# Kernel optimization log

Hardware: AMD Instinct MI355X
Metric: run time of the kernel (lower is better)

Reference implementation:

```python
import jax, jax.numpy as jnp
import numpy as np

EPS = 1e-6  # epsilon used to snap near-zero plane distances (Moller-style robustness)


def _interval(p, d):
    """Interval of the intersection line covered by a triangle.
    p: [..., 3] projections of the 3 vertices onto the intersection-line axis.
    d: [..., 3] signed distances of the 3 vertices to the other triangle's plane.
    Returns (tmin, tmax); invalid (non-straddling) -> (+inf, -inf).
    """
    nxt = jnp.array([1, 2, 0])
    di, dj = d, d[..., nxt]
    pi, pj = p, p[..., nxt]
    # edge crosses the plane iff endpoint distances have opposite signs
    # (or exactly one endpoint lies on the plane)
    valid = (di * dj <= 0) & ~((di == 0) & (dj == 0))
    denom = di - dj
    t = pi + (pj - pi) * di / jnp.where(denom == 0, 1.0, denom)
    tmin = jnp.min(jnp.where(valid, t, jnp.inf), axis=-1)
    tmax = jnp.max(jnp.where(valid, t, -jnp.inf), axis=-1)
    return tmin, tmax


def _pairwise_intersect(T):
    """Moller-style triangle-triangle intersection test for all N^2 pairs.
    T: [N, 3, 3] triangle soup. Returns bool [N, N].
    """
    N = T.shape[0]
    n = jnp.cross(T[:, 1] - T[:, 0], T[:, 2] - T[:, 0])   # [N,3] plane normals
    d = -jnp.sum(n * T[:, 0], axis=-1)                      # [N] plane offsets
    # signed distances: verts of triangle b to plane of triangle u (dv), and vice versa (du)
    dv = jnp.einsum('bvc,nc->bnv', T, n) + d[None, :, None]  # [N,N,3]
    du = jnp.einsum('nvc,bc->bnv', T, n) + d[:, None, None]  # [N,N,3]
    dv = jnp.where(jnp.abs(dv) < EPS, 0.0, dv)
    du = jnp.where(jnp.abs(du) < EPS, 0.0, du)
    # all vertices strictly on one side -> no intersection
    ssv = jnp.all(dv > 0, -1) | jnp.all(dv < 0, -1)
    ssu = jnp.all(du > 0, -1) | jnp.all(du < 0, -1)
    # direction of plane-plane intersection line; project onto its dominant axis
    D = jnp.cross(n[:, None, :], n[None, :, :])              # [N,N,3]
    ax = jnp.argmax(jnp.abs(D), axis=-1)                     # [N,N]
    idx = jnp.broadcast_to(ax[..., None, None], (N, N, 3, 1))
    pv = jnp.take_along_axis(jnp.broadcast_to(T[:, None], (N, N, 3, 3)), idx, -1)[..., 0]
    pu = jnp.take_along_axis(jnp.broadcast_to(T[None, :], (N, N, 3, 3)), idx, -1)[..., 0]
    t0v, t1v = _interval(pv, dv)
    t0u, t1u = _interval(pu, du)
    overlap = jnp.maximum(t0v, t0u) <= jnp.minimum(t1v, t1u)
    return ~ssv & ~ssu & overlap


def setup_inputs() -> dict:
    key = jax.random.key(0)
    triangles = jax.random.normal(key, (2048, 3, 3), dtype=jnp.float32)
    return {"triangles": triangles}


def reference(triangles):
    # CPU extension produces the strictly-upper-triangular pairwise matrix;
    # the torch wrapper symmetrizes it and adds the identity.
    N = triangles.shape[0]
    M = _pairwise_intersect(triangles).astype(jnp.float32)
    S = jnp.triu(M, 1)
    return S + S.T + jnp.eye(N, dtype=jnp.float32)
```

## Files before the change

kernel.cpp:

```cpp
#include <hip/hip_runtime.h>
#include <math.h>


static constexpr float EPS_SNAP = 1e-6f;

__device__ __forceinline__ float snapz(float x) {
    return (fabsf(x) < EPS_SNAP) ? 0.0f : x;
}

__device__ __forceinline__ void tri_interval(const float p[3], const float d[3],
                                             float& tmin, float& tmax) {
#pragma clang fp contract(off)
    tmin = INFINITY;
    tmax = -INFINITY;
#pragma unroll
    for (int e = 0; e < 3; ++e) {
        const int i0 = e;
        const int i1 = (e + 1) % 3;
        const float di = d[i0], dj = d[i1];
        const float pi = p[i0], pj = p[i1];
        const bool valid = (di * dj <= 0.0f) && !((di == 0.0f) && (dj == 0.0f));
        const float denom = di - dj;
        const float dsafe = (denom == 0.0f) ? 1.0f : denom;
        const float t = pi + ((pj - pi) * di) / dsafe;
        if (valid) {
            tmin = fminf(tmin, t);
            tmax = fmaxf(tmax, t);
        }
    }
}

__global__ __launch_bounds__(256) void tri_pairs_kernel(
    const float* __restrict__ tri, float* __restrict__ out, int n)
{
#pragma clang fp contract(off)
    const int j = blockIdx.x * 64 + threadIdx.x;
    const int i = blockIdx.y * 4 + threadIdx.y;
    if (i >= n || j >= n) return;

    const float* __restrict__ A = tri + (size_t)i * 9;
    const float* __restrict__ B = tri + (size_t)j * 9;

    float Av[9], Bv[9];
#pragma unroll
    for (int k = 0; k < 9; ++k) { Av[k] = A[k]; Bv[k] = B[k]; }

    const float ae1x = Av[3] - Av[0], ae1y = Av[4] - Av[1], ae1z = Av[5] - Av[2];
    const float ae2x = Av[6] - Av[0], ae2y = Av[7] - Av[1], ae2z = Av[8] - Av[2];
    const float nax = ae1y * ae2z - ae1z * ae2y;
    const float nay = ae1z * ae2x - ae1x * ae2z;
    const float naz = ae1x * ae2y - ae1y * ae2x;
    const float da = -(((nax * Av[0]) + (nay * Av[1])) + (naz * Av[2]));

    const float be1x = Bv[3] - Bv[0], be1y = Bv[4] - Bv[1], be1z = Bv[5] - Bv[2];
    const float be2x = Bv[6] - Bv[0], be2y = Bv[7] - Bv[1], be2z = Bv[8] - Bv[2];
    const float nbx = be1y * be2z - be1z * be2y;
    const float nby = be1z * be2x - be1x * be2z;
    const float nbz = be1x * be2y - be1y * be2x;
    const float db = -(((nbx * Bv[0]) + (nby * Bv[1])) + (nbz * Bv[2]));

    float dv[3], du[3];
#pragma unroll
    for (int v = 0; v < 3; ++v) {
        dv[v] = snapz((((Av[3 * v] * nbx) + (Av[3 * v + 1] * nby)) + (Av[3 * v + 2] * nbz)) + db);
        du[v] = snapz((((Bv[3 * v] * nax) + (Bv[3 * v + 1] * nay)) + (Bv[3 * v + 2] * naz)) + da);
    }

    const bool ssv = (dv[0] > 0.0f && dv[1] > 0.0f && dv[2] > 0.0f) ||
                     (dv[0] < 0.0f && dv[1] < 0.0f && dv[2] < 0.0f);
    const bool ssu = (du[0] > 0.0f && du[1] > 0.0f && du[2] > 0.0f) ||
                     (du[0] < 0.0f && du[1] < 0.0f && du[2] < 0.0f);

    const float Dx = nay * nbz - naz * nby;
    const float Dy = naz * nbx - nax * nbz;
    const float Dz = nax * nby - nay * nbx;
    const float m0 = fabsf(Dx), m1 = fabsf(Dy), m2 = fabsf(Dz);
    int axm = 0;
    float mm = m0;
    if (m1 > mm) { axm = 1; mm = m1; }
    if (m2 > mm) { axm = 2; }

    float pv[3], pu[3];
#pragma unroll
    for (int v = 0; v < 3; ++v) {
        const float a0 = Av[3 * v], a1 = Av[3 * v + 1], a2 = Av[3 * v + 2];
        const float b0 = Bv[3 * v], b1 = Bv[3 * v + 1], b2 = Bv[3 * v + 2];
        pv[v] = (axm == 0) ? a0 : ((axm == 1) ? a1 : a2);
        pu[v] = (axm == 0) ? b0 : ((axm == 1) ? b1 : b2);
    }

    float t0v, t1v, t0u, t1u;
    tri_interval(pv, dv, t0v, t1v);
    tri_interval(pu, du, t0u, t1u);

    const bool overlap = fmaxf(t0v, t0u) <= fminf(t1v, t1u);
    const bool hit = (!ssv) && (!ssu) && overlap;

    float r = hit ? 1.0f : 0.0f;
    if (i == j) r = 1.0f;
    out[(size_t)i * n + j] = r;
}

extern "C" void kernel_launch(void* const* d_in, const int* in_sizes, int n_in,
                              void* d_out, int out_size, void* d_ws, size_t ws_size,
                              hipStream_t stream) {
    const float* tri = (const float*)d_in[0];
    float* out = (float*)d_out;
    const int n = in_sizes[0] / 9;

    dim3 block(64, 4);
    dim3 grid((n + 63) / 64, (n + 3) / 4);
    tri_pairs_kernel<<<grid, block, 0, stream>>>(tri, out, n);
}
```

Before: 86.21 us.

## Precompute plane normals, tile pairs with symmetry and transpose-write lower half

Adds a pre-pass kernel that computes each triangle's plane normal and offset once into workspace. The pair kernel now processes 32x32 tiles, stages the row triangles in shared memory, and evaluates only upper-triangular tiles. It writes each result tile and its transpose through shared memory with float4 stores. This roughly halves the per-pair arithmetic and removes the redundant normal recomputation, at the cost of an extra launch and a grid where half the blocks exit immediately. It assumes n is a multiple of 32 and that the pair test is symmetric.

```diff
diff --git a/kernel.cpp b/kernel.cpp
--- a/kernel.cpp
+++ b/kernel.cpp
@@ -3,6 +3,7 @@
 
 
 static constexpr float EPS_SNAP = 1e-6f;
+static constexpr int TS = 32;
 
 __device__ __forceinline__ float snapz(float x) {
     return (fabsf(x) < EPS_SNAP) ? 0.0f : x;
@@ -30,75 +31,124 @@
     }
 }
 
-__global__ __launch_bounds__(256) void tri_pairs_kernel(
-    const float* __restrict__ tri, float* __restrict__ out, int n)
+__global__ __launch_bounds__(256) void plane_kernel(
+    const float* __restrict__ tri, float4* __restrict__ planes, int n)
 {
 #pragma clang fp contract(off)
-    const int j = blockIdx.x * 64 + threadIdx.x;
-    const int i = blockIdx.y * 4 + threadIdx.y;
-    if (i >= n || j >= n) return;
+    const int i = blockIdx.x * 256 + threadIdx.x;
+    if (i >= n) return;
+    const float* A = tri + (size_t)i * 9;
+    float Av[9];
+#pragma unroll
+    for (int k = 0; k < 9; ++k) Av[k] = A[k];
+    const float e1x = Av[3] - Av[0], e1y = Av[4] - Av[1], e1z = Av[5] - Av[2];
+    const float e2x = Av[6] - Av[0], e2y = Av[7] - Av[1], e2z = Av[8] - Av[2];
+    const float nx = e1y * e2z - e1z * e2y;
+    const float ny = e1z * e2x - e1x * e2z;
+    const float nz = e1x * e2y - e1y * e2x;
+    const float d = -(((nx * Av[0]) + (ny * Av[1])) + (nz * Av[2]));
+    planes[i] = make_float4(nx, ny, nz, d);
+}
 
-    const float* __restrict__ A = tri + (size_t)i * 9;
-    const float* __restrict__ B = tri + (size_t)j * 9;
+__global__ __launch_bounds__(256) void tile_kernel(
+    const float* __restrict__ tri, const float4* __restrict__ planes,
+    float* __restrict__ out, int n)
+{
+#pragma clang fp contract(off)
+    const int tc = blockIdx.x, tr = blockIdx.y;
+    if (tr > tc) return;
+    const int C = tc * TS, R = tr * TS;
 
-    float Av[9], Bv[9];
+    __shared__ float As[TS][13];
+    __shared__ float Sres[TS][TS + 1];
+
+    const int tx = threadIdx.x;
+    const int t = threadIdx.y * 32 + tx;
+
+    if (t < TS) {
+        const float* a = tri + (size_t)(R + t) * 9;
 #pragma unroll
-    for (int k = 0; k < 9; ++k) { Av[k] = A[k]; Bv[k] = B[k]; }
-
-    const float ae1x = Av[3] - Av[0], ae1y = Av[4] - Av[1], ae1z = Av[5] - Av[2];
-    const float ae2x = Av[6] - Av[0], ae2y = Av[7] - Av[1], ae2z = Av[8] - Av[2];
-    const float nax = ae1y * ae2z - ae1z * ae2y;
-    const float nay = ae1z * ae2x - ae1x * ae2z;
-    const float naz = ae1x * ae2y - ae1y * ae2x;
-    const float da = -(((nax * Av[0]) + (nay * Av[1])) + (naz * Av[2]));
-
-    const float be1x = Bv[3] - Bv[0], be1y = Bv[4] - Bv[1], be1z = Bv[5] - Bv[2];
-    const float be2x = Bv[6] - Bv[0], be2y = Bv[7] - Bv[1], be2z = Bv[8] - Bv[2];
-    const float nbx = be1y * be2z - be1z * be2y;
-    const float nby = be1z * be2x - be1x * be2z;
-    const float nbz = be1x * be2y - be1y * be2x;
-    const float db = -(((nbx * Bv[0]) + (nby * Bv[1])) + (nbz * Bv[2]));
-
-    float dv[3], du[3];
-#pragma unroll
-    for (int v = 0; v < 3; ++v) {
-        dv[v] = snapz((((Av[3 * v] * nbx) + (Av[3 * v + 1] * nby)) + (Av[3 * v + 2] * nbz)) + db);
-        du[v] = snapz((((Bv[3 * v] * nax) + (Bv[3 * v + 1] * nay)) + (Bv[3 * v + 2] * naz)) + da);
+        for (int k = 0; k < 9; ++k) As[t][k] = a[k];
+        const float4 p = planes[R + t];
+        As[t][9] = p.x; As[t][10] = p.y; As[t][11] = p.z; As[t][12] = p.w;
     }
 
-    const bool ssv = (dv[0] > 0.0f && dv[1] > 0.0f && dv[2] > 0.0f) ||
-                     (dv[0] < 0.0f && dv[1] < 0.0f && dv[2] < 0.0f);
-    const bool ssu = (du[0] > 0.0f && du[1] > 0.0f && du[2] > 0.0f) ||
-                     (du[0] < 0.0f && du[1] < 0.0f && du[2] < 0.0f);
+    const int j = C + tx;
+    const float* b = tri + (size_t)j * 9;
+    float Bv[9];
+#pragma unroll
+    for (int k = 0; k < 9; ++k) Bv[k] = b[k];
+    const float4 pb = planes[j];
+    const float nbx = pb.x, nby = pb.y, nbz = pb.z, db = pb.w;
 
-    const float Dx = nay * nbz - naz * nby;
-    const float Dy = naz * nbx - nax * nbz;
-    const float Dz = nax * nby - nay * nbx;
-    const float m0 = fabsf(Dx), m1 = fabsf(Dy), m2 = fabsf(Dz);
-    int axm = 0;
-    float mm = m0;
-    if (m1 > mm) { axm = 1; mm = m1; }
-    if (m2 > mm) { axm = 2; }
+    __syncthreads();
 
-    float pv[3], pu[3];
 #pragma unroll
-    for (int v = 0; v < 3; ++v) {
-        const float a0 = Av[3 * v], a1 = Av[3 * v + 1], a2 = Av[3 * v + 2];
-        const float b0 = Bv[3 * v], b1 = Bv[3 * v + 1], b2 = Bv[3 * v + 2];
-        pv[v] = (axm == 0) ? a0 : ((axm == 1) ? a1 : a2);
-        pu[v] = (axm == 0) ? b0 : ((axm == 1) ? b1 : b2);
+    for (int kk = 0; kk < 4; ++kk) {
+        const int r = threadIdx.y + 8 * kk;
+        const int i = R + r;
+
+        float Av[9];
+#pragma unroll
+        for (int k = 0; k < 9; ++k) Av[k] = As[r][k];
+        const float nax = As[r][9], nay = As[r][10], naz = As[r][11], da = As[r][12];
+
+        float dv[3], du[3];
+#pragma unroll
+        for (int v = 0; v < 3; ++v) {
+            dv[v] = snapz((((Av[3 * v] * nbx) + (Av[3 * v + 1] * nby)) + (Av[3 * v + 2] * nbz)) + db);
+            du[v] = snapz((((Bv[3 * v] * nax) + (Bv[3 * v + 1] * nay)) + (Bv[3 * v + 2] * naz)) + da);
+        }
+
+        const bool ssv = (dv[0] > 0.0f && dv[1] > 0.0f && dv[2] > 0.0f) ||
+                         (dv[0] < 0.0f && dv[1] < 0.0f && dv[2] < 0.0f);
+        const bool ssu = (du[0] > 0.0f && du[1] > 0.0f && du[2] > 0.0f) ||
+                         (du[0] < 0.0f && du[1] < 0.0f && du[2] < 0.0f);
+
+        const float Dx = nay * nbz - naz * nby;
+        const float Dy = naz * nbx - nax * nbz;
+        const float Dz = nax * nby - nay * nbx;
+        const float m0 = fabsf(Dx), m1 = fabsf(Dy), m2 = fabsf(Dz);
+        int axm = 0;
+        float mm = m0;
+        if (m1 > mm) { axm = 1; mm = m1; }
+        if (m2 > mm) { axm = 2; }
+
+        float pv[3], pu[3];
+#pragma unroll
+        for (int v = 0; v < 3; ++v) {
+            pv[v] = (axm == 0) ? Av[3 * v] : ((axm == 1) ? Av[3 * v + 1] : Av[3 * v + 2]);
+            pu[v] = (axm == 0) ? Bv[3 * v] : ((axm == 1) ? Bv[3 * v + 1] : Bv[3 * v + 2]);
+        }
+
+        float t0v, t1v, t0u, t1u;
+        tri_interval(pv, dv, t0v, t1v);
+        tri_interval(pu, du, t0u, t1u);
+
+        const bool overlap = fmaxf(t0v, t0u) <= fminf(t1v, t1u);
+        const bool hit = (!ssv) && (!ssu) && overlap;
+
+        float res = hit ? 1.0f : 0.0f;
+        if (i == j) res = 1.0f;
+        Sres[r][tx] = res;
     }
 
-    float t0v, t1v, t0u, t1u;
-    tri_interval(pv, dv, t0v, t1v);
-    tri_interval(pu, du, t0u, t1u);
+    __syncthreads();
 
-    const bool overlap = fmaxf(t0v, t0u) <= fminf(t1v, t1u);
-    const bool hit = (!ssv) && (!ssu) && overlap;
-
-    float r = hit ? 1.0f : 0.0f;
-    if (i == j) r = 1.0f;
-    out[(size_t)i * n + j] = r;
+    {
+        const int row = t >> 3;
+        const int c4 = (t & 7) * 4;
+        float4 v;
+        v.x = Sres[row][c4 + 0]; v.y = Sres[row][c4 + 1];
+        v.z = Sres[row][c4 + 2]; v.w = Sres[row][c4 + 3];
+        *(float4*)&out[(size_t)(R + row) * n + C + c4] = v;
+        if (tr != tc) {
+            float4 w;
+            w.x = Sres[c4 + 0][row]; w.y = Sres[c4 + 1][row];
+            w.z = Sres[c4 + 2][row]; w.w = Sres[c4 + 3][row];
+            *(float4*)&out[(size_t)(C + row) * n + R + c4] = w;
+        }
+    }
 }
 
 extern "C" void kernel_launch(void* const* d_in, const int* in_sizes, int n_in,
@@ -107,8 +157,11 @@
     const float* tri = (const float*)d_in[0];
     float* out = (float*)d_out;
     const int n = in_sizes[0] / 9;
+    float4* planes = (float4*)d_ws;
 
-    dim3 block(64, 4);
-    dim3 grid((n + 63) / 64, (n + 3) / 4);
-    tri_pairs_kernel<<<grid, block, 0, stream>>>(tri, out, n);
+    plane_kernel<<<(n + 255) / 256, 256, 0, stream>>>(tri, planes, n);
+
+    dim3 block(32, 8);
+    dim3 grid(n / TS, n / TS);
+    tile_kernel<<<grid, block, 0, stream>>>(tri, planes, out, n);
 }
```

Result: faster. 78.63 us (-8.8%).
